# Kernel tuning notes

Hardware: AMD Instinct MI355X
Metric: run time of the kernel (lower is better)

Reference implementation:

```python
import jax, jax.numpy as jnp
import numpy as np

N_NODES = 100000
N_EDGES = 3200000
IN_FEAT = 128


def gcn_conv(x, src, dst, W, b, num_nodes):
    # PyG GCNConv: h = x @ W, then symmetric-normalized aggregation with self-loops.
    h = x @ W  # [N, out]
    # add self loops
    loop = jnp.arange(num_nodes, dtype=src.dtype)
    s = jnp.concatenate([src, loop])
    d = jnp.concatenate([dst, loop])
    # degree over destination (col) with unit edge weights
    deg = jax.ops.segment_sum(jnp.ones_like(s, dtype=h.dtype), d, num_segments=num_nodes)
    dinv = jnp.where(deg > 0, jax.lax.rsqrt(deg), 0.0)
    norm = dinv[s] * dinv[d]  # [E+N]
    msg = norm[:, None] * h[s]  # gather source features, scale per edge
    out = jax.ops.segment_sum(msg, d, num_segments=num_nodes)
    return out + b


def setup_inputs() -> dict:
    key = jax.random.key(0)
    ks = jax.random.split(key, 8)
    x = jax.random.normal(ks[0], (N_NODES, IN_FEAT), dtype=jnp.float32)
    edge_index = jax.random.randint(ks[1], (2, N_EDGES), 0, N_NODES, dtype=jnp.int64)
    def glorot(k, shape):
        lim = np.sqrt(6.0 / (shape[0] + shape[1]))
        return jax.random.uniform(k, shape, jnp.float32, -lim, lim)
    return {
        "x": x,
        "edge_index": edge_index,
        "W1": glorot(ks[2], (IN_FEAT, 4)), "b1": jnp.zeros((4,), jnp.float32),
        "W2": glorot(ks[3], (4, 2)),       "b2": jnp.zeros((2,), jnp.float32),
        "W3": glorot(ks[4], (2, 1)),       "b3": jnp.zeros((1,), jnp.float32),
    }


def reference(x, edge_index, W1, b1, W2, b2, W3, b3):
    src, dst = edge_index[0], edge_index[1]
    n = x.shape[0]
    h = gcn_conv(x, src, dst, W1, b1, n)
    h = jax.nn.relu(h)
    # F.dropout(training=self.training): inference mode -> identity
    h = gcn_conv(h, src, dst, W2, b2, n)
    h = jax.nn.relu(h)
    h = gcn_conv(h, src, dst, W3, b3, n)
    return jax.nn.sigmoid(h)  # [N, 1]
```

## Files before the change

### kernel.cpp

```cpp
#include <hip/hip_runtime.h>
#include <math.h>


#define TPB 256
#define CHUNK 4096
#define EPT (CHUNK / TPB)
#define SLAB2 9216
#define NSMAX 1024

__global__ __launch_bounds__(TPB) void k_part(
    const int* __restrict__ src, const int* __restrict__ dst,
    unsigned int* __restrict__ slab, int* __restrict__ lstartT,
    int NB, int NBP, int NS, int E)
{
    __shared__ int hist[512];
    __shared__ int wtot[4];
    __shared__ unsigned int sorted[CHUNK];
    int t = threadIdx.x;
    int base = blockIdx.x * CHUNK;
    int n = min(CHUNK, E - base);
    hist[t] = 0; hist[t + 256] = 0;
    __syncthreads();
    unsigned int meta[EPT];
#pragma unroll
    for (int k = 0; k < EPT; ++k) {
        int li = k * TPB + t;
        if (li < n) {
            int d = dst[base + li];
            int lp = atomicAdd(&hist[d >> 8], 1);
            meta[k] = ((unsigned)d << 13) | (unsigned)lp;
        } else meta[k] = 0xFFFFFFFFu;
    }
    __syncthreads();
    int v0 = hist[2 * t], v1 = hist[2 * t + 1];
    int pr = v0 + v1;
    int x = pr;
    int lane = t & 63;
    for (int d = 1; d < 64; d <<= 1) {
        int y = __shfl_up(x, d);
        if (lane >= d) x += y;
    }
    if (lane == 63) wtot[t >> 6] = x;
    __syncthreads();
    int w = t >> 6;
    int woff = 0;
#pragma unroll
    for (int i = 0; i < 4; ++i) if (i < w) woff += wtot[i];
    int excl = woff + x - pr;
    hist[2 * t] = excl;
    hist[2 * t + 1] = excl + v0;
    __syncthreads();
#pragma unroll
    for (int k = 0; k < EPT; ++k) {
        if (meta[k] != 0xFFFFFFFFu) {
            unsigned m = meta[k];
            int d = (int)(m >> 13);
            int lp = (int)(m & 0x1FFFu);
            unsigned pk = (unsigned)src[base + k * TPB + t] | ((unsigned)(d & 255) << 17);
            sorted[hist[d >> 8] + lp] = pk;
        }
    }
    __syncthreads();
    const uint4* s4 = (const uint4*)sorted;
    uint4* g4 = (uint4*)(slab + (size_t)base);
    for (int i = t; i < CHUNK / 4; i += TPB) g4[i] = s4[i];
    for (int i = t; i < NBP; i += TPB)
        lstartT[(size_t)i * NS + blockIdx.x] = (i < NB) ? hist[i] : n;
}

__global__ __launch_bounds__(TPB) void k_degree(
    const unsigned int* __restrict__ slab, const int* __restrict__ lstartT,
    int* __restrict__ ssrc, int2* __restrict__ oc, float* __restrict__ dinv,
    const float* __restrict__ x, const float* __restrict__ W1,
    float* __restrict__ h1, int NS, int NB, int N)
{
    __shared__ unsigned int pl[SLAB2];
    __shared__ int sstart[NSMAX];
    __shared__ int slen[NSMAX];
    __shared__ int c[TPB];
    __shared__ int cur[TPB];
    __shared__ int wtot[4];
    int t = threadIdx.x;

    if (blockIdx.x >= NB) {
        float* Ws = (float*)pl;
        for (int i = t; i < 512; i += TPB) Ws[i] = W1[i];
        __syncthreads();
        int tt = (blockIdx.x - NB) * TPB + t;
        int v = tt >> 2, p = tt & 3;
        if (v >= N) return;
        const float4* xr = (const float4*)(x + (size_t)v * 128);
        float a0 = 0.f, a1 = 0.f, a2 = 0.f, a3 = 0.f;
#pragma unroll
        for (int i = 0; i < 8; ++i) {
            int cc = p + i * 4;
            float4 xx = xr[cc];
            const float* wv = &Ws[cc * 16];
            a0 += xx.x * wv[0] + xx.y * wv[4] + xx.z * wv[8]  + xx.w * wv[12];
            a1 += xx.x * wv[1] + xx.y * wv[5] + xx.z * wv[9]  + xx.w * wv[13];
            a2 += xx.x * wv[2] + xx.y * wv[6] + xx.z * wv[10] + xx.w * wv[14];
            a3 += xx.x * wv[3] + xx.y * wv[7] + xx.z * wv[11] + xx.w * wv[15];
        }
        a0 += __shfl_xor(a0, 1); a0 += __shfl_xor(a0, 2);
        a1 += __shfl_xor(a1, 1); a1 += __shfl_xor(a1, 2);
        a2 += __shfl_xor(a2, 1); a2 += __shfl_xor(a2, 2);
        a3 += __shfl_xor(a3, 1); a3 += __shfl_xor(a3, 2);
        if (p == 0) ((float4*)h1)[v] = make_float4(a0, a1, a2, a3);
        return;
    }

    int b = blockIdx.x;
    c[t] = 0;
    for (int j = t; j < NSMAX; j += TPB) {
        int st = 0, len = 0;
        if (j < NS) {
            st = lstartT[(size_t)b * NS + j];
            len = lstartT[(size_t)(b + 1) * NS + j] - st;
        }
        sstart[j] = st;
        slen[j] = len;
    }
    __syncthreads();
    int s0 = slen[4 * t], s1 = slen[4 * t + 1], s2 = slen[4 * t + 2], s3 = slen[4 * t + 3];
    int pq = s0 + s1 + s2 + s3;
    int xs = pq;
    int lane = t & 63;
    for (int d = 1; d < 64; d <<= 1) {
        int y = __shfl_up(xs, d);
        if (lane >= d) xs += y;
    }
    if (lane == 63) wtot[t >> 6] = xs;
    __syncthreads();
    int w = t >> 6;
    int woff = 0, tot = 0;
#pragma unroll
    for (int i = 0; i < 4; ++i) { int z = wtot[i]; tot += z; if (i < w) woff += z; }
    int e0 = woff + xs - pq;
    slen[4 * t]     = e0;
    slen[4 * t + 1] = e0 + s0;
    slen[4 * t + 2] = e0 + s0 + s1;
    slen[4 * t + 3] = e0 + s0 + s1 + s2;
    __syncthreads();
    int total = min(tot, SLAB2);
    int g = t >> 3, l = t & 7;
    for (int j0 = 0; j0 < NS; j0 += 32) {
        int j = j0 + g;
        if (j < NS) {
            int lo = slen[j];
            int len = slen[j + 1] - lo;
            int lim = min(len, SLAB2 - lo);
            const unsigned int* sp = slab + (size_t)j * CHUNK + sstart[j];
            for (int k = l; k < lim; k += 8) pl[lo + k] = sp[k];
        }
    }
    __syncthreads();
    for (int i = t; i < total; i += TPB) atomicAdd(&c[(pl[i] >> 17) & 255], 1);
    __syncthreads();
    int cv = c[t];
    int xc = cv;
    for (int d = 1; d < 64; d <<= 1) {
        int y = __shfl_up(xc, d);
        if (lane >= d) xc += y;
    }
    if (lane == 63) wtot[t >> 6] = xc;
    __syncthreads();
    int woff2 = 0;
#pragma unroll
    for (int i = 0; i < 4; ++i) if (i < w) woff2 += wtot[i];
    int excl = woff2 + xc - cv;
    int v = (b << 8) + t;
    if (v < N) {
        oc[v] = make_int2(b * SLAB2 + excl, cv);
        dinv[v] = rsqrtf((float)(cv + 1));
    }
    cur[t] = excl;
    __syncthreads();
    int* sb = ssrc + (size_t)b * SLAB2;
    for (int i = t; i < total; i += TPB) {
        unsigned pk = pl[i];
        int pos = atomicAdd(&cur[(pk >> 17) & 255], 1);
        sb[pos] = (int)(pk & 0x1FFFFu);
    }
}

__global__ __launch_bounds__(TPB) void k_gather1(
    const int2* __restrict__ oc, const int* __restrict__ ssrc,
    const float* __restrict__ h1, const float* __restrict__ dinv,
    const float* __restrict__ b1, const float* __restrict__ W2,
    float* __restrict__ hs2, int n) {
    int t = blockIdx.x * TPB + threadIdx.x;
    int v = t >> 3, p = t & 7;
    if (v >= n) return;
    int2 ocv = oc[v];
    int base = ocv.x, c = ocv.y;
    float4 acc = make_float4(0.f, 0.f, 0.f, 0.f);
    for (int i = p; i < c; i += 8) {
        int s = ssrc[base + i];
        float ds = dinv[s];
        float4 h = ((const float4*)h1)[s];
        acc.x += __fmul_rn(ds, h.x);
        acc.y += __fmul_rn(ds, h.y);
        acc.z += __fmul_rn(ds, h.z);
        acc.w += __fmul_rn(ds, h.w);
    }
    acc.x += __shfl_xor(acc.x, 1); acc.x += __shfl_xor(acc.x, 2); acc.x += __shfl_xor(acc.x, 4);
    acc.y += __shfl_xor(acc.y, 1); acc.y += __shfl_xor(acc.y, 2); acc.y += __shfl_xor(acc.y, 4);
    acc.z += __shfl_xor(acc.z, 1); acc.z += __shfl_xor(acc.z, 2); acc.z += __shfl_xor(acc.z, 4);
    acc.w += __shfl_xor(acc.w, 1); acc.w += __shfl_xor(acc.w, 2); acc.w += __shfl_xor(acc.w, 4);
    if (p == 0) {
        float di = dinv[v];
        float4 hv = ((const float4*)h1)[v];
        float h0 = __fmul_rn(di, hv.x);
        float h1v = __fmul_rn(di, hv.y);
        float h2 = __fmul_rn(di, hv.z);
        float h3 = __fmul_rn(di, hv.w);
        float o0 = fmaxf(di * (acc.x + h0)  + b1[0], 0.f);
        float o1 = fmaxf(di * (acc.y + h1v) + b1[1], 0.f);
        float o2 = fmaxf(di * (acc.z + h2)  + b1[2], 0.f);
        float o3 = fmaxf(di * (acc.w + h3)  + b1[3], 0.f);
        float g0 = o0 * W2[0] + o1 * W2[2] + o2 * W2[4] + o3 * W2[6];
        float g1 = o0 * W2[1] + o1 * W2[3] + o2 * W2[5] + o3 * W2[7];
        ((float2*)hs2)[v] = make_float2(di * g0, di * g1);
    }
}

__global__ __launch_bounds__(TPB) void k_gather2(
    const int2* __restrict__ oc, const int* __restrict__ ssrc,
    const float* __restrict__ hs2, const float* __restrict__ dinv,
    const float* __restrict__ b2, const float* __restrict__ W3,
    float* __restrict__ hs3, int n) {
    int t = blockIdx.x * TPB + threadIdx.x;
    int v = t >> 3, p = t & 7;
    if (v >= n) return;
    int2 ocv = oc[v];
    int base = ocv.x, c = ocv.y;
    float2 acc = make_float2(0.f, 0.f);
    for (int i = p; i < c; i += 8) {
        int s = ssrc[base + i];
        float2 h = ((const float2*)hs2)[s];
        acc.x += h.x; acc.y += h.y;
    }
    acc.x += __shfl_xor(acc.x, 1); acc.x += __shfl_xor(acc.x, 2); acc.x += __shfl_xor(acc.x, 4);
    acc.y += __shfl_xor(acc.y, 1); acc.y += __shfl_xor(acc.y, 2); acc.y += __shfl_xor(acc.y, 4);
    if (p == 0) {
        float2 hv = ((const float2*)hs2)[v];
        float di = dinv[v];
        float o0 = fmaxf(di * (acc.x + hv.x) + b2[0], 0.f);
        float o1 = fmaxf(di * (acc.y + hv.y) + b2[1], 0.f);
        float h3 = o0 * W3[0] + o1 * W3[1];
        hs3[v] = di * h3;
    }
}

__global__ __launch_bounds__(TPB) void k_gather3(
    const int2* __restrict__ oc, const int* __restrict__ ssrc,
    const float* __restrict__ hs3, const float* __restrict__ dinv,
    const float* __restrict__ b3, float* __restrict__ out, int n) {
    int t = blockIdx.x * TPB + threadIdx.x;
    int v = t >> 3, p = t & 7;
    if (v >= n) return;
    int2 ocv = oc[v];
    int base = ocv.x, c = ocv.y;
    float acc = 0.f;
    for (int i = p; i < c; i += 8) acc += hs3[ssrc[base + i]];
    acc += __shfl_xor(acc, 1); acc += __shfl_xor(acc, 2); acc += __shfl_xor(acc, 4);
    if (p == 0) {
        float di = dinv[v];
        float agg = di * (acc + hs3[v]) + b3[0];
        out[v] = 1.0f / (1.0f + __expf(-agg));
    }
}

extern "C" void kernel_launch(void* const* d_in, const int* in_sizes, int n_in,
                              void* d_out, int out_size, void* d_ws, size_t ws_size,
                              hipStream_t stream) {
    const float* x  = (const float*)d_in[0];
    const int* ei   = (const int*)d_in[1];
    const float* W1 = (const float*)d_in[2];
    const float* b1 = (const float*)d_in[3];
    const float* W2 = (const float*)d_in[4];
    const float* b2 = (const float*)d_in[5];
    const float* W3 = (const float*)d_in[6];
    const float* b3 = (const float*)d_in[7];
    float* out = (float*)d_out;

    const int N = in_sizes[0] / 128;
    const int E = in_sizes[1] / 2;
    const int* src = ei;
    const int* dst = ei + E;

    const int NS  = (E + CHUNK - 1) / CHUNK;
    const int NB  = (N + 255) >> 8;
    const int NBP = NB + 1;

    char* w = (char*)d_ws;
    auto carve = [&](size_t bytes) { char* p = w; w += (bytes + 15) & ~(size_t)15; return p; };
    unsigned int* slab = (unsigned int*)carve((size_t)NS * CHUNK * 4);
    int* lstartT       = (int*)carve((size_t)NBP * NS * 4);
    int* ssrc          = (int*)carve((size_t)NB * SLAB2 * 4);
    int2* oc           = (int2*)carve((size_t)N * 8);
    float* dinv        = (float*)carve((size_t)N * 4);
    float* h1          = (float*)carve((size_t)4 * N * 4);
    float* hs2 = (float*)slab;
    float* hs3 = hs2 + (size_t)2 * N;

    const int nb1  = (4 * N + TPB - 1) / TPB;
    const int nbN8 = (8 * N + TPB - 1) / TPB;

    k_part   <<<NS, TPB, 0, stream>>>(src, dst, slab, lstartT, NB, NBP, NS, E);
    k_degree <<<NB + nb1, TPB, 0, stream>>>(slab, lstartT, ssrc, oc, dinv, x, W1, h1, NS, NB, N);
    k_gather1<<<nbN8, TPB, 0, stream>>>(oc, ssrc, h1, dinv, b1, W2, hs2, N);
    k_gather2<<<nbN8, TPB, 0, stream>>>(oc, ssrc, hs2, dinv, b2, W3, hs3, N);
    k_gather3<<<nbN8, TPB, 0, stream>>>(oc, ssrc, hs3, dinv, b3, out, N);
}
```

Before: 222.2 us.

## Halve destination buckets, move x@W1 into partition kernel, prescale h1 by dinv

Destination buckets shrink from 256 to 128 nodes, which doubles the number of degree/CSR blocks and reduces per-block shared memory. The per-segment slab copy becomes a per-element binary search over segment offsets. The dense x@W1 projection moves from the degree kernel into the partition kernel, so it can overlap with edge partitioning. The degree kernel now writes dinv-prescaled features (hs1), which lets gather1 skip the per-edge dinv[s] load, at the cost of an extra N×4 buffer write.

```diff
diff --git a/kernel.cpp b/kernel.cpp
--- a/kernel.cpp
+++ b/kernel.cpp
@@ -5,21 +5,52 @@
 #define TPB 256
 #define CHUNK 4096
 #define EPT (CHUNK / TPB)
-#define SLAB2 9216
+#define BSZ 128
+#define SLAB2 4992
 #define NSMAX 1024
 
 __global__ __launch_bounds__(TPB) void k_part(
     const int* __restrict__ src, const int* __restrict__ dst,
     unsigned int* __restrict__ slab, int* __restrict__ lstartT,
-    int NB, int NBP, int NS, int E)
+    const float* __restrict__ x, const float* __restrict__ W1,
+    float* __restrict__ h1,
+    int NB, int NS, int E, int N)
 {
-    __shared__ int hist[512];
+    __shared__ int hist[NSMAX];
+    __shared__ unsigned int sorted[CHUNK];
     __shared__ int wtot[4];
-    __shared__ unsigned int sorted[CHUNK];
     int t = threadIdx.x;
+
+    if (blockIdx.x >= NS) {
+        float* Ws = (float*)sorted;
+        for (int i = t; i < 512; i += TPB) Ws[i] = W1[i];
+        __syncthreads();
+        int tt = (blockIdx.x - NS) * TPB + t;
+        int v = tt >> 2, p = tt & 3;
+        if (v >= N) return;
+        const float4* xr = (const float4*)(x + (size_t)v * 128);
+        float a0 = 0.f, a1 = 0.f, a2 = 0.f, a3 = 0.f;
+#pragma unroll
+        for (int i = 0; i < 8; ++i) {
+            int cc = p + i * 4;
+            float4 xx = xr[cc];
+            const float* wv = &Ws[cc * 16];
+            a0 += xx.x*wv[0] + xx.y*wv[4] + xx.z*wv[8]  + xx.w*wv[12];
+            a1 += xx.x*wv[1] + xx.y*wv[5] + xx.z*wv[9]  + xx.w*wv[13];
+            a2 += xx.x*wv[2] + xx.y*wv[6] + xx.z*wv[10] + xx.w*wv[14];
+            a3 += xx.x*wv[3] + xx.y*wv[7] + xx.z*wv[11] + xx.w*wv[15];
+        }
+        a0 += __shfl_xor(a0,1); a0 += __shfl_xor(a0,2);
+        a1 += __shfl_xor(a1,1); a1 += __shfl_xor(a1,2);
+        a2 += __shfl_xor(a2,1); a2 += __shfl_xor(a2,2);
+        a3 += __shfl_xor(a3,1); a3 += __shfl_xor(a3,2);
+        if (p == 0) ((float4*)h1)[v] = make_float4(a0, a1, a2, a3);
+        return;
+    }
+
     int base = blockIdx.x * CHUNK;
     int n = min(CHUNK, E - base);
-    hist[t] = 0; hist[t + 256] = 0;
+    for (int i = t; i < NSMAX; i += TPB) hist[i] = 0;
     __syncthreads();
     unsigned int meta[EPT];
 #pragma unroll
@@ -27,28 +58,25 @@
         int li = k * TPB + t;
         if (li < n) {
             int d = dst[base + li];
-            int lp = atomicAdd(&hist[d >> 8], 1);
+            int lp = atomicAdd(&hist[d >> 7], 1);
             meta[k] = ((unsigned)d << 13) | (unsigned)lp;
         } else meta[k] = 0xFFFFFFFFu;
     }
     __syncthreads();
-    int v0 = hist[2 * t], v1 = hist[2 * t + 1];
-    int pr = v0 + v1;
-    int x = pr;
-    int lane = t & 63;
-    for (int d = 1; d < 64; d <<= 1) {
-        int y = __shfl_up(x, d);
-        if (lane >= d) x += y;
-    }
-    if (lane == 63) wtot[t >> 6] = x;
-    __syncthreads();
-    int w = t >> 6;
+    int lane = t & 63, w = t >> 6;
+    int q0 = hist[4*t], q1 = hist[4*t+1], q2 = hist[4*t+2], q3 = hist[4*t+3];
+    int pq = q0 + q1 + q2 + q3, xs = pq;
+    for (int d = 1; d < 64; d <<= 1) { int y = __shfl_up(xs, d); if (lane >= d) xs += y; }
+    if (lane == 63) wtot[w] = xs;
+    __syncthreads();
     int woff = 0;
 #pragma unroll
     for (int i = 0; i < 4; ++i) if (i < w) woff += wtot[i];
-    int excl = woff + x - pr;
-    hist[2 * t] = excl;
-    hist[2 * t + 1] = excl + v0;
+    int e0 = woff + xs - pq;
+    hist[4*t]   = e0;
+    hist[4*t+1] = e0 + q0;
+    hist[4*t+2] = e0 + q0 + q1;
+    hist[4*t+3] = e0 + q0 + q1 + q2;
     __syncthreads();
 #pragma unroll
     for (int k = 0; k < EPT; ++k) {
@@ -56,136 +84,103 @@
             unsigned m = meta[k];
             int d = (int)(m >> 13);
             int lp = (int)(m & 0x1FFFu);
-            unsigned pk = (unsigned)src[base + k * TPB + t] | ((unsigned)(d & 255) << 17);
-            sorted[hist[d >> 8] + lp] = pk;
+            unsigned pk = (unsigned)src[base + k*TPB + t] | ((unsigned)(d & 127) << 17);
+            sorted[hist[d >> 7] + lp] = pk;
         }
     }
     __syncthreads();
     const uint4* s4 = (const uint4*)sorted;
     uint4* g4 = (uint4*)(slab + (size_t)base);
     for (int i = t; i < CHUNK / 4; i += TPB) g4[i] = s4[i];
-    for (int i = t; i < NBP; i += TPB)
-        lstartT[(size_t)i * NS + blockIdx.x] = (i < NB) ? hist[i] : n;
+    for (int i = t; i < NB + 1; i += TPB)
+        lstartT[(size_t)i * NS + blockIdx.x] = hist[i];
 }
 
 __global__ __launch_bounds__(TPB) void k_degree(
     const unsigned int* __restrict__ slab, const int* __restrict__ lstartT,
     int* __restrict__ ssrc, int2* __restrict__ oc, float* __restrict__ dinv,
-    const float* __restrict__ x, const float* __restrict__ W1,
-    float* __restrict__ h1, int NS, int NB, int N)
+    const float* __restrict__ h1, float* __restrict__ hs1,
+    int NS, int NB, int N)
 {
     __shared__ unsigned int pl[SLAB2];
     __shared__ int sstart[NSMAX];
     __shared__ int slen[NSMAX];
-    __shared__ int c[TPB];
-    __shared__ int cur[TPB];
+    __shared__ int c[BSZ];
+    __shared__ int cur[BSZ];
     __shared__ int wtot[4];
-    int t = threadIdx.x;
-
-    if (blockIdx.x >= NB) {
-        float* Ws = (float*)pl;
-        for (int i = t; i < 512; i += TPB) Ws[i] = W1[i];
-        __syncthreads();
-        int tt = (blockIdx.x - NB) * TPB + t;
-        int v = tt >> 2, p = tt & 3;
-        if (v >= N) return;
-        const float4* xr = (const float4*)(x + (size_t)v * 128);
-        float a0 = 0.f, a1 = 0.f, a2 = 0.f, a3 = 0.f;
-#pragma unroll
-        for (int i = 0; i < 8; ++i) {
-            int cc = p + i * 4;
-            float4 xx = xr[cc];
-            const float* wv = &Ws[cc * 16];
-            a0 += xx.x * wv[0] + xx.y * wv[4] + xx.z * wv[8]  + xx.w * wv[12];
-            a1 += xx.x * wv[1] + xx.y * wv[5] + xx.z * wv[9]  + xx.w * wv[13];
-            a2 += xx.x * wv[2] + xx.y * wv[6] + xx.z * wv[10] + xx.w * wv[14];
-            a3 += xx.x * wv[3] + xx.y * wv[7] + xx.z * wv[11] + xx.w * wv[15];
-        }
-        a0 += __shfl_xor(a0, 1); a0 += __shfl_xor(a0, 2);
-        a1 += __shfl_xor(a1, 1); a1 += __shfl_xor(a1, 2);
-        a2 += __shfl_xor(a2, 1); a2 += __shfl_xor(a2, 2);
-        a3 += __shfl_xor(a3, 1); a3 += __shfl_xor(a3, 2);
-        if (p == 0) ((float4*)h1)[v] = make_float4(a0, a1, a2, a3);
-        return;
-    }
-
-    int b = blockIdx.x;
-    c[t] = 0;
+    int t = threadIdx.x, b = blockIdx.x;
+    if (t < BSZ) c[t] = 0;
     for (int j = t; j < NSMAX; j += TPB) {
         int st = 0, len = 0;
         if (j < NS) {
-            st = lstartT[(size_t)b * NS + j];
+            st  = lstartT[(size_t)b * NS + j];
             len = lstartT[(size_t)(b + 1) * NS + j] - st;
         }
         sstart[j] = st;
         slen[j] = len;
     }
     __syncthreads();
-    int s0 = slen[4 * t], s1 = slen[4 * t + 1], s2 = slen[4 * t + 2], s3 = slen[4 * t + 3];
-    int pq = s0 + s1 + s2 + s3;
-    int xs = pq;
-    int lane = t & 63;
-    for (int d = 1; d < 64; d <<= 1) {
-        int y = __shfl_up(xs, d);
-        if (lane >= d) xs += y;
-    }
-    if (lane == 63) wtot[t >> 6] = xs;
-    __syncthreads();
-    int w = t >> 6;
+    int lane = t & 63, w = t >> 6;
+    int s0 = slen[4*t], s1 = slen[4*t+1], s2 = slen[4*t+2], s3 = slen[4*t+3];
+    int pq = s0 + s1 + s2 + s3, xs = pq;
+    for (int d = 1; d < 64; d <<= 1) { int y = __shfl_up(xs, d); if (lane >= d) xs += y; }
+    if (lane == 63) wtot[w] = xs;
+    __syncthreads();
     int woff = 0, tot = 0;
 #pragma unroll
     for (int i = 0; i < 4; ++i) { int z = wtot[i]; tot += z; if (i < w) woff += z; }
     int e0 = woff + xs - pq;
-    slen[4 * t]     = e0;
-    slen[4 * t + 1] = e0 + s0;
-    slen[4 * t + 2] = e0 + s0 + s1;
-    slen[4 * t + 3] = e0 + s0 + s1 + s2;
+    slen[4*t]   = e0;
+    slen[4*t+1] = e0 + s0;
+    slen[4*t+2] = e0 + s0 + s1;
+    slen[4*t+3] = e0 + s0 + s1 + s2;
     __syncthreads();
     int total = min(tot, SLAB2);
-    int g = t >> 3, l = t & 7;
-    for (int j0 = 0; j0 < NS; j0 += 32) {
-        int j = j0 + g;
-        if (j < NS) {
-            int lo = slen[j];
-            int len = slen[j + 1] - lo;
-            int lim = min(len, SLAB2 - lo);
-            const unsigned int* sp = slab + (size_t)j * CHUNK + sstart[j];
-            for (int k = l; k < lim; k += 8) pl[lo + k] = sp[k];
-        }
-    }
-    __syncthreads();
-    for (int i = t; i < total; i += TPB) atomicAdd(&c[(pl[i] >> 17) & 255], 1);
-    __syncthreads();
-    int cv = c[t];
+    for (int i = t; i < total; i += TPB) {
+        int lo = 0, hi = NS;
+        while (hi - lo > 1) {
+            int mid = (lo + hi) >> 1;
+            bool le = (slen[mid] <= i);
+            lo = le ? mid : lo;
+            hi = le ? hi : mid;
+        }
+        pl[i] = slab[(size_t)lo * CHUNK + sstart[lo] + (i - slen[lo])];
+    }
+    __syncthreads();
+    for (int i = t; i < total; i += TPB) atomicAdd(&c[(pl[i] >> 17) & 127], 1);
+    __syncthreads();
+    int cv = (t < BSZ) ? c[t] : 0;
     int xc = cv;
-    for (int d = 1; d < 64; d <<= 1) {
-        int y = __shfl_up(xc, d);
-        if (lane >= d) xc += y;
-    }
-    if (lane == 63) wtot[t >> 6] = xc;
+    for (int d = 1; d < 64; d <<= 1) { int y = __shfl_up(xc, d); if (lane >= d) xc += y; }
+    if (lane == 63) wtot[w] = xc;
     __syncthreads();
     int woff2 = 0;
 #pragma unroll
     for (int i = 0; i < 4; ++i) if (i < w) woff2 += wtot[i];
     int excl = woff2 + xc - cv;
-    int v = (b << 8) + t;
-    if (v < N) {
-        oc[v] = make_int2(b * SLAB2 + excl, cv);
-        dinv[v] = rsqrtf((float)(cv + 1));
-    }
-    cur[t] = excl;
+    if (t < BSZ) {
+        int v = (b << 7) + t;
+        if (v < N) {
+            oc[v] = make_int2(b * SLAB2 + excl, cv);
+            float di = rsqrtf((float)(cv + 1));
+            dinv[v] = di;
+            float4 hv = ((const float4*)h1)[v];
+            ((float4*)hs1)[v] = make_float4(di*hv.x, di*hv.y, di*hv.z, di*hv.w);
+        }
+        cur[t] = excl;
+    }
     __syncthreads();
     int* sb = ssrc + (size_t)b * SLAB2;
     for (int i = t; i < total; i += TPB) {
         unsigned pk = pl[i];
-        int pos = atomicAdd(&cur[(pk >> 17) & 255], 1);
+        int pos = atomicAdd(&cur[(pk >> 17) & 127], 1);
         sb[pos] = (int)(pk & 0x1FFFFu);
     }
 }
 
 __global__ __launch_bounds__(TPB) void k_gather1(
     const int2* __restrict__ oc, const int* __restrict__ ssrc,
-    const float* __restrict__ h1, const float* __restrict__ dinv,
+    const float* __restrict__ hs1, const float* __restrict__ dinv,
     const float* __restrict__ b1, const float* __restrict__ W2,
     float* __restrict__ hs2, int n) {
     int t = blockIdx.x * TPB + threadIdx.x;
@@ -196,28 +191,20 @@
     float4 acc = make_float4(0.f, 0.f, 0.f, 0.f);
     for (int i = p; i < c; i += 8) {
         int s = ssrc[base + i];
-        float ds = dinv[s];
-        float4 h = ((const float4*)h1)[s];
-        acc.x += __fmul_rn(ds, h.x);
-        acc.y += __fmul_rn(ds, h.y);
-        acc.z += __fmul_rn(ds, h.z);
-        acc.w += __fmul_rn(ds, h.w);
+        float4 h = ((const float4*)hs1)[s];
+        acc.x += h.x; acc.y += h.y; acc.z += h.z; acc.w += h.w;
     }
     acc.x += __shfl_xor(acc.x, 1); acc.x += __shfl_xor(acc.x, 2); acc.x += __shfl_xor(acc.x, 4);
     acc.y += __shfl_xor(acc.y, 1); acc.y += __shfl_xor(acc.y, 2); acc.y += __shfl_xor(acc.y, 4);
     acc.z += __shfl_xor(acc.z, 1); acc.z += __shfl_xor(acc.z, 2); acc.z += __shfl_xor(acc.z, 4);
     acc.w += __shfl_xor(acc.w, 1); acc.w += __shfl_xor(acc.w, 2); acc.w += __shfl_xor(acc.w, 4);
     if (p == 0) {
+        float4 hv = ((const float4*)hs1)[v];
         float di = dinv[v];
-        float4 hv = ((const float4*)h1)[v];
-        float h0 = __fmul_rn(di, hv.x);
-        float h1v = __fmul_rn(di, hv.y);
-        float h2 = __fmul_rn(di, hv.z);
-        float h3 = __fmul_rn(di, hv.w);
-        float o0 = fmaxf(di * (acc.x + h0)  + b1[0], 0.f);
-        float o1 = fmaxf(di * (acc.y + h1v) + b1[1], 0.f);
-        float o2 = fmaxf(di * (acc.z + h2)  + b1[2], 0.f);
-        float o3 = fmaxf(di * (acc.w + h3)  + b1[3], 0.f);
+        float o0 = fmaxf(di * (acc.x + hv.x) + b1[0], 0.f);
+        float o1 = fmaxf(di * (acc.y + hv.y) + b1[1], 0.f);
+        float o2 = fmaxf(di * (acc.z + hv.z) + b1[2], 0.f);
+        float o3 = fmaxf(di * (acc.w + hv.w) + b1[3], 0.f);
         float g0 = o0 * W2[0] + o1 * W2[2] + o2 * W2[4] + o3 * W2[6];
         float g1 = o0 * W2[1] + o1 * W2[3] + o2 * W2[5] + o3 * W2[7];
         ((float2*)hs2)[v] = make_float2(di * g0, di * g1);
@@ -289,27 +276,27 @@
     const int* src = ei;
     const int* dst = ei + E;
 
-    const int NS  = (E + CHUNK - 1) / CHUNK;
-    const int NB  = (N + 255) >> 8;
-    const int NBP = NB + 1;
+    const int NS = (E + CHUNK - 1) / CHUNK;
+    const int NB = (N + BSZ - 1) / BSZ;
 
     char* w = (char*)d_ws;
     auto carve = [&](size_t bytes) { char* p = w; w += (bytes + 15) & ~(size_t)15; return p; };
     unsigned int* slab = (unsigned int*)carve((size_t)NS * CHUNK * 4);
-    int* lstartT       = (int*)carve((size_t)NBP * NS * 4);
+    int* lstartT       = (int*)carve((size_t)(NB + 1) * NS * 4);
     int* ssrc          = (int*)carve((size_t)NB * SLAB2 * 4);
     int2* oc           = (int2*)carve((size_t)N * 8);
     float* dinv        = (float*)carve((size_t)N * 4);
     float* h1          = (float*)carve((size_t)4 * N * 4);
-    float* hs2 = (float*)slab;
-    float* hs3 = hs2 + (size_t)2 * N;
+    float* hs1         = (float*)carve((size_t)4 * N * 4);
+    float* hs2         = (float*)carve((size_t)2 * N * 4);
+    float* hs3         = (float*)carve((size_t)N * 4);
 
     const int nb1  = (4 * N + TPB - 1) / TPB;
     const int nbN8 = (8 * N + TPB - 1) / TPB;
 
-    k_part   <<<NS, TPB, 0, stream>>>(src, dst, slab, lstartT, NB, NBP, NS, E);
-    k_degree <<<NB + nb1, TPB, 0, stream>>>(slab, lstartT, ssrc, oc, dinv, x, W1, h1, NS, NB, N);
-    k_gather1<<<nbN8, TPB, 0, stream>>>(oc, ssrc, h1, dinv, b1, W2, hs2, N);
+    k_part   <<<NS + nb1, TPB, 0, stream>>>(src, dst, slab, lstartT, x, W1, h1, NB, NS, E, N);
+    k_degree <<<NB, TPB, 0, stream>>>(slab, lstartT, ssrc, oc, dinv, h1, hs1, NS, NB, N);
+    k_gather1<<<nbN8, TPB, 0, stream>>>(oc, ssrc, hs1, dinv, b1, W2, hs2, N);
     k_gather2<<<nbN8, TPB, 0, stream>>>(oc, ssrc, hs2, dinv, b2, W3, hs3, N);
     k_gather3<<<nbN8, TPB, 0, stream>>>(oc, ssrc, hs3, dinv, b3, out, N);
 }
```

Result: faster. 217.7 us (-2.0%).
